# Kernel tuning notes

Hardware: AMD Instinct MI355X
Metric: run time of the kernel (lower is better)

Reference implementation:

```python
import jax, jax.numpy as jnp
import numpy as np

# Static config matching init_kwargs
SPATIAL_SCALE = 0.25
SAMPLING_RATIO = 2
PH, PW = 7, 7
ALIGNED = True
CLOCKWISE = False


def setup_inputs() -> dict:
    key = jax.random.key(0)
    k_feat, k_b, k_c, k_wh, k_a = jax.random.split(key, 5)
    N, C, H, W = 2, 256, 256, 256
    n_rois = 1024
    feat = jax.random.normal(k_feat, (N, C, H, W), dtype=jnp.float32)
    # rois: (batch_idx, cx, cy, w, h, angle) in IMAGE coordinates (stride-4 map)
    b = jax.random.randint(k_b, (n_rois,), 0, N).astype(jnp.float32)
    ctr = jax.random.uniform(k_c, (n_rois, 2), minval=0.0, maxval=1024.0)
    wh = jax.random.uniform(k_wh, (n_rois, 2), minval=32.0, maxval=320.0)
    ang = jax.random.uniform(k_a, (n_rois,), minval=-np.pi, maxval=np.pi)
    rois = jnp.concatenate([b[:, None], ctr, wh, ang[:, None]], axis=1).astype(jnp.float32)
    return {"input": feat, "rois": rois}


def _roi_align_rotated(feat, rois):
    N, C, H, W = feat.shape
    b = rois[:, 0].astype(jnp.int32)
    off = 0.5 if ALIGNED else 0.0
    cx = rois[:, 1] * SPATIAL_SCALE - off
    cy = rois[:, 2] * SPATIAL_SCALE - off
    rw = rois[:, 3] * SPATIAL_SCALE
    rh = rois[:, 4] * SPATIAL_SCALE
    th = -rois[:, 5] if CLOCKWISE else rois[:, 5]
    if not ALIGNED:
        rw = jnp.maximum(rw, 1.0)
        rh = jnp.maximum(rh, 1.0)
    bin_h = rh / PH  # [n]
    bin_w = rw / PW
    gh = gw = SAMPLING_RATIO  # sampling_ratio > 0 -> static grid

    py = jnp.arange(PH, dtype=feat.dtype)
    px = jnp.arange(PW, dtype=feat.dtype)
    sy = (jnp.arange(gh, dtype=feat.dtype) + 0.5) / gh
    sx = (jnp.arange(gw, dtype=feat.dtype) + 0.5) / gw
    # roi-local sample coords: yy [n,PH,gh], xx [n,PW,gw]
    yy = (-rh / 2)[:, None, None] + (py[None, :, None] + sy[None, None, :]) * bin_h[:, None, None]
    xx = (-rw / 2)[:, None, None] + (px[None, :, None] + sx[None, None, :]) * bin_w[:, None, None]
    # broadcast to [n,PH,PW,gh,gw]
    yy5 = yy[:, :, None, :, None]
    xx5 = xx[:, None, :, None, :]
    cos = jnp.cos(th)[:, None, None, None, None]
    sin = jnp.sin(th)[:, None, None, None, None]
    cyb = cy[:, None, None, None, None]
    cxb = cx[:, None, None, None, None]
    # mmcv convention: y = yy*cos - xx*sin + cy ; x = yy*sin + xx*cos + cx
    y = yy5 * cos - xx5 * sin + cyb
    x = yy5 * sin + xx5 * cos + cxb

    valid = (y > -1.0) & (y < H) & (x > -1.0) & (x < W)
    y = jnp.maximum(y, 0.0)
    x = jnp.maximum(x, 0.0)
    yl = y.astype(jnp.int32)
    xl = x.astype(jnp.int32)
    condy = yl >= H - 1
    condx = xl >= W - 1
    yl = jnp.where(condy, H - 1, yl)
    xl = jnp.where(condx, W - 1, xl)
    yh = jnp.minimum(yl + 1, H - 1)
    xh = jnp.minimum(xl + 1, W - 1)
    y = jnp.where(condy, yl.astype(y.dtype), y)
    x = jnp.where(condx, xl.astype(x.dtype), x)
    ly = y - yl
    lx = x - xl
    hy = 1.0 - ly
    hx = 1.0 - lx

    b5 = b[:, None, None, None, None]

    def gather(yi, xi):
        # -> [n,PH,PW,gh,gw,C]
        return feat[b5, :, yi, xi]

    v = ((hy * hx)[..., None] * gather(yl, xl)
         + (hy * lx)[..., None] * gather(yl, xh)
         + (ly * hx)[..., None] * gather(yh, xl)
         + (ly * lx)[..., None] * gather(yh, xh))
    v = jnp.where(valid[..., None], v, 0.0)
    out = v.mean(axis=(3, 4))  # average over the gh*gw samples -> [n,PH,PW,C]
    return jnp.transpose(out, (0, 3, 1, 2))  # [n,C,PH,PW]


def reference(input, rois):
    return _roi_align_rotated(input, rois)
```

## Files before the change

kernel.cpp:

```cpp
#include <hip/hip_runtime.h>

#define SPATIAL_SCALE 0.25f
#define PH_ 7
#define PW_ 7
#define NBINS 49
#define NSAMP 196
#define C_ 256
#define H_ 256
#define W_ 256
#define HW_ (H_ * W_)
#define RES_STRIDE 257

__global__ __launch_bounds__(256) void transpose_nchw_nhwc(
    const float* __restrict__ in, float* __restrict__ out) {
  __shared__ float tile[32][33];
  const int b  = blockIdx.z;
  const int c0 = blockIdx.y * 32;
  const int p0 = blockIdx.x * 32;
  const float* src = in  + (size_t)b * C_ * HW_;
  float*       dst = out + (size_t)b * HW_ * C_;
  const int tx = threadIdx.x;
  const int ty = threadIdx.y;
#pragma unroll
  for (int i = 0; i < 32; i += 8)
    tile[ty + i][tx] = src[(size_t)(c0 + ty + i) * HW_ + p0 + tx];
  __syncthreads();
#pragma unroll
  for (int i = 0; i < 32; i += 8)
    dst[(size_t)(p0 + ty + i) * C_ + c0 + tx] = tile[tx][ty + i];
}

template <bool NHWC>
__global__ __launch_bounds__(256) void roi_align_rotated_kernel(
    const float* __restrict__ feat, const float* __restrict__ rois,
    float* __restrict__ out) {
  __shared__ int4   d_off[NSAMP];
  __shared__ float4 d_w[NSAMP];
  __shared__ float  res[NBINS * RES_STRIDE];

  const int r = blockIdx.x;
  const int t = threadIdx.x;

  if (t < NSAMP) {
    const float* rp = rois + r * 6;
    const int   b  = (int)rp[0];
    const float cx = rp[1] * SPATIAL_SCALE - 0.5f;
    const float cy = rp[2] * SPATIAL_SCALE - 0.5f;
    const float rw = rp[3] * SPATIAL_SCALE;
    const float rh = rp[4] * SPATIAL_SCALE;
    const float th = rp[5];
    float sn, cs;
    sincosf(th, &sn, &cs);
    const float bin_h = rh / (float)PH_;
    const float bin_w = rw / (float)PW_;

    const int s   = t;
    const int bin = s >> 2;
    const int sub = s & 3;
    const int ph  = bin / 7;
    const int pw  = bin - ph * 7;
    const int iy  = sub >> 1;
    const int ix  = sub & 1;

    const float yy = -0.5f * rh + ((float)ph + ((float)iy + 0.5f) * 0.5f) * bin_h;
    const float xx = -0.5f * rw + ((float)pw + ((float)ix + 0.5f) * 0.5f) * bin_w;
    float y = yy * cs - xx * sn + cy;
    float x = yy * sn + xx * cs + cx;

    const bool valid = (y > -1.0f) && (y < (float)H_) &&
                       (x > -1.0f) && (x < (float)W_);
    y = fminf(fmaxf(y, 0.0f), (float)(H_ - 1));
    x = fminf(fmaxf(x, 0.0f), (float)(W_ - 1));
    const int yl = (int)y;
    const int xl = (int)x;
    const int yh = min(yl + 1, H_ - 1);
    const int xh = min(xl + 1, W_ - 1);
    const float ly = y - (float)yl, lx = x - (float)xl;
    const float hy = 1.0f - ly, hx = 1.0f - lx;
    float w11 = hy * hx, w12 = hy * lx, w21 = ly * hx, w22 = ly * lx;
    if (!valid) { w11 = w12 = w21 = w22 = 0.0f; }

    int4 off;
    if (NHWC) {
      off.x = ((b * H_ + yl) * W_ + xl) * C_;
      off.y = ((b * H_ + yl) * W_ + xh) * C_;
      off.z = ((b * H_ + yh) * W_ + xl) * C_;
      off.w = ((b * H_ + yh) * W_ + xh) * C_;
    } else {
      const int base = b * C_ * HW_;
      off.x = base + yl * W_ + xl;
      off.y = base + yl * W_ + xh;
      off.z = base + yh * W_ + xl;
      off.w = base + yh * W_ + xh;
    }
    d_off[s] = off;
    d_w[s]   = make_float4(w11, w12, w21, w22);
  }
  __syncthreads();

  const int c    = t;
  const int coff = NHWC ? c : c * HW_;
  for (int bin = 0; bin < NBINS; ++bin) {
    float acc = 0.0f;
#pragma unroll
    for (int sub = 0; sub < 4; ++sub) {
      const int4   o = d_off[bin * 4 + sub];
      const float4 w = d_w[bin * 4 + sub];
      acc += w.x * feat[o.x + coff];
      acc += w.y * feat[o.y + coff];
      acc += w.z * feat[o.z + coff];
      acc += w.w * feat[o.w + coff];
    }
    res[bin * RES_STRIDE + c] = acc * 0.25f;
  }
  __syncthreads();

  float* outr = out + (size_t)r * (C_ * NBINS);
#pragma unroll 1
  for (int i = t; i < C_ * NBINS; i += 256) {
    const int cc = i / NBINS;
    const int bb = i - cc * NBINS;
    outr[i] = res[bb * RES_STRIDE + cc];
  }
}

extern "C" void kernel_launch(void* const* d_in, const int* in_sizes, int n_in,
                              void* d_out, int out_size, void* d_ws, size_t ws_size,
                              hipStream_t stream) {
  const float* feat = (const float*)d_in[0];
  const float* rois = (const float*)d_in[1];
  float* out = (float*)d_out;
  const int n_rois  = in_sizes[1] / 6;
  const int n_batch = in_sizes[0] / (C_ * HW_);

  const size_t need = (size_t)n_batch * C_ * HW_ * sizeof(float);
  if (ws_size >= need) {
    float* feat_t = (float*)d_ws;
    dim3 tb(32, 8);
    dim3 tg(HW_ / 32, C_ / 32, n_batch);
    hipLaunchKernelGGL(transpose_nchw_nhwc, tg, tb, 0, stream, feat, feat_t);
    hipLaunchKernelGGL((roi_align_rotated_kernel<true>), dim3(n_rois), dim3(256),
                       0, stream, feat_t, rois, out);
  } else {
    hipLaunchKernelGGL((roi_align_rotated_kernel<false>), dim3(n_rois), dim3(256),
                       0, stream, feat, rois, out);
  }
}
```

Before: 315.8 us.

## Vectorize transpose with 64x64 tiles and compress ROI sample metadata in shared memory

The NCHW-to-NHWC transpose now uses 64x64 tiles with float4 global loads and stores, replacing scalar 32x32 tiles, to cut the instruction count of the bandwidth-bound transpose. The NHWC ROI kernel packs the four corner offsets into one int with edge flags and stores the bilinear weights as half2. It uses an XOR-swizzled result buffer instead of a padded one and requests 3 blocks per CU, all to shrink shared memory and raise occupancy. Half-precision weights add rounding error, which may matter for tolerance.

```diff
diff --git a/kernel.cpp b/kernel.cpp
--- a/kernel.cpp
+++ b/kernel.cpp
@@ -1,4 +1,5 @@
 #include <hip/hip_runtime.h>
+#include <hip/hip_fp16.h>
 
 #define SPATIAL_SCALE 0.25f
 #define PH_ 7
@@ -9,34 +10,45 @@
 #define H_ 256
 #define W_ 256
 #define HW_ (H_ * W_)
-#define RES_STRIDE 257
 
 __global__ __launch_bounds__(256) void transpose_nchw_nhwc(
     const float* __restrict__ in, float* __restrict__ out) {
-  __shared__ float tile[32][33];
+  __shared__ float tile[64 * 68];
   const int b  = blockIdx.z;
-  const int c0 = blockIdx.y * 32;
-  const int p0 = blockIdx.x * 32;
-  const float* src = in  + (size_t)b * C_ * HW_;
-  float*       dst = out + (size_t)b * HW_ * C_;
-  const int tx = threadIdx.x;
-  const int ty = threadIdx.y;
+  const int p0 = blockIdx.x * 64;
+  const int c0 = blockIdx.y * 64;
+  const int t  = threadIdx.x;
+  const int i  = t & 15;
+  const int q  = t >> 4;
+
+  const float* src = in + (size_t)b * C_ * HW_ + (size_t)(c0 + 4 * q) * HW_
+                        + (p0 + 4 * i);
+  const float4 r0 = *(const float4*)(src + 0 * HW_);
+  const float4 r1 = *(const float4*)(src + 1 * HW_);
+  const float4 r2 = *(const float4*)(src + 2 * HW_);
+  const float4 r3 = *(const float4*)(src + 3 * HW_);
+
+  float* tp = &tile[(4 * i) * 68 + 4 * q];
+  *(float4*)(tp + 0 * 68) = make_float4(r0.x, r1.x, r2.x, r3.x);
+  *(float4*)(tp + 1 * 68) = make_float4(r0.y, r1.y, r2.y, r3.y);
+  *(float4*)(tp + 2 * 68) = make_float4(r0.z, r1.z, r2.z, r3.z);
+  *(float4*)(tp + 3 * 68) = make_float4(r0.w, r1.w, r2.w, r3.w);
+  __syncthreads();
+
+  float* dst = out + (size_t)b * HW_ * C_ + (size_t)(p0 + q) * C_ + (c0 + 4 * i);
 #pragma unroll
-  for (int i = 0; i < 32; i += 8)
-    tile[ty + i][tx] = src[(size_t)(c0 + ty + i) * HW_ + p0 + tx];
-  __syncthreads();
-#pragma unroll
-  for (int i = 0; i < 32; i += 8)
-    dst[(size_t)(p0 + ty + i) * C_ + c0 + tx] = tile[tx][ty + i];
-}
-
-template <bool NHWC>
-__global__ __launch_bounds__(256) void roi_align_rotated_kernel(
+  for (int k = 0; k < 4; ++k) {
+    const float4 v = *(const float4*)&tile[(16 * k + q) * 68 + 4 * i];
+    *(float4*)(dst + (size_t)(16 * k) * C_) = v;
+  }
+}
+
+__global__ __launch_bounds__(256, 3) void roi_align_rotated_nhwc(
     const float* __restrict__ feat, const float* __restrict__ rois,
     float* __restrict__ out) {
-  __shared__ int4   d_off[NSAMP];
-  __shared__ float4 d_w[NSAMP];
-  __shared__ float  res[NBINS * RES_STRIDE];
+  __shared__ int     d_off[NSAMP];
+  __shared__ __half2 d_w[NSAMP * 2];
+  __shared__ float   res[NBINS * 256];
 
   const int r = blockIdx.x;
   const int t = threadIdx.x;
@@ -48,15 +60,13 @@
     const float cy = rp[2] * SPATIAL_SCALE - 0.5f;
     const float rw = rp[3] * SPATIAL_SCALE;
     const float rh = rp[4] * SPATIAL_SCALE;
-    const float th = rp[5];
     float sn, cs;
-    sincosf(th, &sn, &cs);
+    sincosf(rp[5], &sn, &cs);
     const float bin_h = rh / (float)PH_;
     const float bin_w = rw / (float)PW_;
 
-    const int s   = t;
-    const int bin = s >> 2;
-    const int sub = s & 3;
+    const int bin = t >> 2;
+    const int sub = t & 3;
     const int ph  = bin / 7;
     const int pw  = bin - ph * 7;
     const int iy  = sub >> 1;
@@ -73,45 +83,38 @@
     x = fminf(fmaxf(x, 0.0f), (float)(W_ - 1));
     const int yl = (int)y;
     const int xl = (int)x;
-    const int yh = min(yl + 1, H_ - 1);
-    const int xh = min(xl + 1, W_ - 1);
     const float ly = y - (float)yl, lx = x - (float)xl;
     const float hy = 1.0f - ly, hx = 1.0f - lx;
     float w11 = hy * hx, w12 = hy * lx, w21 = ly * hx, w22 = ly * lx;
     if (!valid) { w11 = w12 = w21 = w22 = 0.0f; }
 
-    int4 off;
-    if (NHWC) {
-      off.x = ((b * H_ + yl) * W_ + xl) * C_;
-      off.y = ((b * H_ + yl) * W_ + xh) * C_;
-      off.z = ((b * H_ + yh) * W_ + xl) * C_;
-      off.w = ((b * H_ + yh) * W_ + xh) * C_;
-    } else {
-      const int base = b * C_ * HW_;
-      off.x = base + yl * W_ + xl;
-      off.y = base + yl * W_ + xh;
-      off.z = base + yh * W_ + xl;
-      off.w = base + yh * W_ + xh;
-    }
-    d_off[s] = off;
-    d_w[s]   = make_float4(w11, w12, w21, w22);
-  }
-  __syncthreads();
-
-  const int c    = t;
-  const int coff = NHWC ? c : c * HW_;
+    const int base = ((b * H_ + yl) * W_ + xl) * C_;
+    const int dxf  = (xl < W_ - 1) ? 1 : 0;
+    const int dyf  = (yl < H_ - 1) ? 2 : 0;
+    d_off[t]       = base | dxf | dyf;
+    d_w[2 * t]     = __floats2half2_rn(w11, w12);
+    d_w[2 * t + 1] = __floats2half2_rn(w21, w22);
+  }
+  __syncthreads();
+
+  const int c = t;
   for (int bin = 0; bin < NBINS; ++bin) {
     float acc = 0.0f;
 #pragma unroll
     for (int sub = 0; sub < 4; ++sub) {
-      const int4   o = d_off[bin * 4 + sub];
-      const float4 w = d_w[bin * 4 + sub];
-      acc += w.x * feat[o.x + coff];
-      acc += w.y * feat[o.y + coff];
-      acc += w.z * feat[o.z + coff];
-      acc += w.w * feat[o.w + coff];
+      const int s    = bin * 4 + sub;
+      const int pc   = d_off[s];
+      const int base = (pc & ~255) + c;
+      const int dx   = (pc & 1) ? C_ : 0;
+      const int dy   = (pc & 2) ? (W_ * C_) : 0;
+      const float2 wa = __half22float2(d_w[2 * s]);
+      const float2 wb = __half22float2(d_w[2 * s + 1]);
+      acc += wa.x * feat[base];
+      acc += wa.y * feat[base + dx];
+      acc += wb.x * feat[base + dy];
+      acc += wb.y * feat[base + dx + dy];
     }
-    res[bin * RES_STRIDE + c] = acc * 0.25f;
+    res[bin * 256 + (c ^ (bin & 31))] = acc * 0.25f;
   }
   __syncthreads();
 
@@ -120,7 +123,80 @@
   for (int i = t; i < C_ * NBINS; i += 256) {
     const int cc = i / NBINS;
     const int bb = i - cc * NBINS;
-    outr[i] = res[bb * RES_STRIDE + cc];
+    outr[i] = res[bb * 256 + (cc ^ (bb & 31))];
+  }
+}
+
+__global__ __launch_bounds__(256) void roi_align_rotated_nchw(
+    const float* __restrict__ feat, const float* __restrict__ rois,
+    float* __restrict__ out) {
+  __shared__ int   d_pix[NSAMP];
+  __shared__ int   d_step[NSAMP];
+  __shared__ float4 d_wt[NSAMP];
+  __shared__ float res[NBINS * 257];
+
+  const int r = blockIdx.x;
+  const int t = threadIdx.x;
+  if (t < NSAMP) {
+    const float* rp = rois + r * 6;
+    const int   b  = (int)rp[0];
+    const float cx = rp[1] * SPATIAL_SCALE - 0.5f;
+    const float cy = rp[2] * SPATIAL_SCALE - 0.5f;
+    const float rw = rp[3] * SPATIAL_SCALE;
+    const float rh = rp[4] * SPATIAL_SCALE;
+    float sn, cs;
+    sincosf(rp[5], &sn, &cs);
+    const float bin_h = rh / (float)PH_;
+    const float bin_w = rw / (float)PW_;
+    const int bin = t >> 2, sub = t & 3;
+    const int ph = bin / 7, pw = bin - ph * 7;
+    const int iy = sub >> 1, ix = sub & 1;
+    const float yy = -0.5f * rh + ((float)ph + ((float)iy + 0.5f) * 0.5f) * bin_h;
+    const float xx = -0.5f * rw + ((float)pw + ((float)ix + 0.5f) * 0.5f) * bin_w;
+    float y = yy * cs - xx * sn + cy;
+    float x = yy * sn + xx * cs + cx;
+    const bool valid = (y > -1.0f) && (y < (float)H_) &&
+                       (x > -1.0f) && (x < (float)W_);
+    y = fminf(fmaxf(y, 0.0f), (float)(H_ - 1));
+    x = fminf(fmaxf(x, 0.0f), (float)(W_ - 1));
+    const int yl = (int)y, xl = (int)x;
+    const float ly = y - (float)yl, lx = x - (float)xl;
+    const float hy = 1.0f - ly, hx = 1.0f - lx;
+    float w11 = hy * hx, w12 = hy * lx, w21 = ly * hx, w22 = ly * lx;
+    if (!valid) { w11 = w12 = w21 = w22 = 0.0f; }
+    d_pix[t]  = (b * H_ + yl) * W_ + xl;
+    d_step[t] = ((xl < W_ - 1) ? 1 : 0) | ((yl < H_ - 1) ? 2 : 0);
+    d_wt[t]   = make_float4(w11, w12, w21, w22);
+  }
+  __syncthreads();
+
+  const int c = t;
+  const size_t coff = (size_t)c * HW_;
+  for (int bin = 0; bin < NBINS; ++bin) {
+    float acc = 0.0f;
+#pragma unroll
+    for (int sub = 0; sub < 4; ++sub) {
+      const int s = bin * 4 + sub;
+      const int p = d_pix[s];
+      const int st = d_step[s];
+      const int dx = (st & 1) ? 1 : 0;
+      const int dy = (st & 2) ? W_ : 0;
+      const float4 w = d_wt[s];
+      const int bb = (p / HW_) * C_ * HW_ + (p % HW_);
+      acc += w.x * feat[bb + coff];
+      acc += w.y * feat[bb + coff + dx];
+      acc += w.z * feat[bb + coff + dy];
+      acc += w.w * feat[bb + coff + dx + dy];
+    }
+    res[bin * 257 + c] = acc * 0.25f;
+  }
+  __syncthreads();
+  float* outr = out + (size_t)r * (C_ * NBINS);
+#pragma unroll 1
+  for (int i = t; i < C_ * NBINS; i += 256) {
+    const int cc = i / NBINS;
+    const int bb = i - cc * NBINS;
+    outr[i] = res[bb * 257 + cc];
   }
 }
 
@@ -136,13 +212,12 @@
   const size_t need = (size_t)n_batch * C_ * HW_ * sizeof(float);
   if (ws_size >= need) {
     float* feat_t = (float*)d_ws;
-    dim3 tb(32, 8);
-    dim3 tg(HW_ / 32, C_ / 32, n_batch);
-    hipLaunchKernelGGL(transpose_nchw_nhwc, tg, tb, 0, stream, feat, feat_t);
-    hipLaunchKernelGGL((roi_align_rotated_kernel<true>), dim3(n_rois), dim3(256),
+    dim3 tg(HW_ / 64, C_ / 64, n_batch);
+    hipLaunchKernelGGL(transpose_nchw_nhwc, tg, dim3(256), 0, stream, feat, feat_t);
+    hipLaunchKernelGGL(roi_align_rotated_nhwc, dim3(n_rois), dim3(256),
                        0, stream, feat_t, rois, out);
   } else {
-    hipLaunchKernelGGL((roi_align_rotated_kernel<false>), dim3(n_rois), dim3(256),
+    hipLaunchKernelGGL(roi_align_rotated_nchw, dim3(n_rois), dim3(256),
                        0, stream, feat, rois, out);
   }
 }
```

Result: slower. 323.1 us (+2.3%).
